# Kernel tuning notes

Measured on AMD Instinct MI355X. Metric: run time of the kernel, lower is better.

Reference implementation:

```python
import jax, jax.numpy as jnp
import numpy as np

N_USERS = 100000
N_ITEMS = 50000
N_EDGES = 1000000
D = 64


def setup_inputs() -> dict:
    key = jax.random.key(0)
    ks = jax.random.split(key, 8)
    return {
        "h_user": jax.random.normal(ks[0], (N_USERS, D), dtype=jnp.float32),
        "h_item": jax.random.normal(ks[1], (N_ITEMS, D), dtype=jnp.float32),
        "buy_src": jax.random.randint(ks[2], (N_EDGES,), 0, N_USERS),
        "buy_dst": jax.random.randint(ks[3], (N_EDGES,), 0, N_ITEMS),
        "w_buy": jax.random.uniform(ks[4], (N_EDGES,), dtype=jnp.float32),
        "bought_src": jax.random.randint(ks[5], (N_EDGES,), 0, N_ITEMS),
        "bought_dst": jax.random.randint(ks[6], (N_EDGES,), 0, N_USERS),
        "w_bought": jax.random.uniform(ks[7], (N_EDGES,), dtype=jnp.float32),
    }


def reference(h_user, h_item, buy_src, buy_dst, w_buy, bought_src, bought_dst, w_bought):
    # 'buy' etype: user -> item. message m = h_user[src] * w, reduce sum at item dst.
    msg_buy = h_user[buy_src] * w_buy[:, None]  # [E, D]
    new_item = jax.ops.segment_sum(msg_buy, buy_dst, num_segments=h_item.shape[0])
    # 'bought' etype: item -> user. message m = h_item[src] * w, reduce sum at user dst.
    msg_bought = h_item[bought_src] * w_bought[:, None]  # [E, D]
    new_user = jax.ops.segment_sum(msg_bought, bought_dst, num_segments=h_user.shape[0])
    # multi_update_all cross-reducer 'mean' is identity here: each ntype is written
    # by exactly one etype, so mean over one contribution == the sum itself.
    return (new_user, new_item)
```

## Files before the change

### kernel.cpp

```cpp
#include <hip/hip_runtime.h>


#define DIM 64

#define RB2     64
#define CAP_I   2048
#define CAP_U   1024
#define NBLK_FC 256

#define RB   128
#define CAP  4096
#define NBLK 256

__global__ void zero_u32(unsigned* __restrict__ p, int n) {
    int i = blockIdx.x * blockDim.x + threadIdx.x;
    if (i < n) p[i] = 0u;
}

__global__ void zero_f32(float4* __restrict__ out, long long n4) {
    long long i = (long long)blockIdx.x * blockDim.x + threadIdx.x;
    const long long stride = (long long)gridDim.x * blockDim.x;
    for (; i < n4; i += stride) out[i] = make_float4(0.f, 0.f, 0.f, 0.f);
}

__global__ void conv_bf16(const float4* __restrict__ in, uint4* __restrict__ out,
                          long long n8) {
    long long i = (long long)blockIdx.x * blockDim.x + threadIdx.x;
    const long long stride = (long long)gridDim.x * blockDim.x;
    for (; i < n8; i += stride) {
        const float4 a = in[2 * i];
        const float4 b = in[2 * i + 1];
        const unsigned* pa = (const unsigned*)&a;
        const unsigned* pb = (const unsigned*)&b;
        unsigned r[8];
        #pragma unroll
        for (int k = 0; k < 4; ++k) {
            unsigned u = pa[k];
            r[k] = (u + 0x7FFFu + ((u >> 16) & 1u)) >> 16;
        }
        #pragma unroll
        for (int k = 0; k < 4; ++k) {
            unsigned u = pb[k];
            r[4 + k] = (u + 0x7FFFu + ((u >> 16) & 1u)) >> 16;
        }
        uint4 o;
        o.x = r[0] | (r[1] << 16);
        o.y = r[2] | (r[3] << 16);
        o.z = r[4] | (r[5] << 16);
        o.w = r[6] | (r[7] << 16);
        out[i] = o;
    }
}

__global__ void scatter_both(const float* __restrict__ h_user,
                             const float* __restrict__ h_item,
                             const int* __restrict__ buy_src,
                             const int* __restrict__ buy_dst,
                             const float* __restrict__ w_buy,
                             const int* __restrict__ bought_src,
                             const int* __restrict__ bought_dst,
                             const float* __restrict__ w_bought,
                             float* __restrict__ new_user,
                             float* __restrict__ new_item,
                             int n_buy, int n_total) {
    const int lane = threadIdx.x & 63;
    const int waves_per_block = blockDim.x >> 6;
    int wid = blockIdx.x * waves_per_block + (threadIdx.x >> 6);
    const int nwaves = gridDim.x * waves_per_block;
    for (int e = wid; e < n_total; e += nwaves) {
        const float* h; const int* srcp; const int* dstp; const float* wp;
        float* outp; int idx;
        if (e < n_buy) { h = h_user; srcp = buy_src; dstp = buy_dst; wp = w_buy; outp = new_item; idx = e; }
        else { h = h_item; srcp = bought_src; dstp = bought_dst; wp = w_bought; outp = new_user; idx = e - n_buy; }
        const int s = srcp[idx];
        const int d = dstp[idx];
        const float weight = wp[idx];
        const float v = h[(long long)s * DIM + lane] * weight;
        atomicAdd(outp + (long long)d * DIM + lane, v);
    }
}


__global__ __launch_bounds__(512) void k3_fc(
        const int* __restrict__ buy_src, const int* __restrict__ buy_dst,
        const float* __restrict__ w_buy,
        const int* __restrict__ bought_src, const int* __restrict__ bought_dst,
        const float* __restrict__ w_bought,
        unsigned* __restrict__ cur, uint2* __restrict__ pay,
        int n_buy, int n_total, int g_item, int G, int chunk) {
    extern __shared__ unsigned sh[];
    for (int g = threadIdx.x; g < G; g += blockDim.x) sh[g] = 0u;
    __syncthreads();
    const int start = blockIdx.x * chunk;
    const int end = (start + chunk < n_total) ? start + chunk : n_total;
    for (int i = start + threadIdx.x; i < end; i += blockDim.x) {
        const int g = (i < n_buy) ? (buy_dst[i] >> 6)
                                  : (g_item + (bought_dst[i - n_buy] >> 6));
        atomicAdd(&sh[g], 1u);
    }
    __syncthreads();
    for (int g = threadIdx.x; g < G; g += blockDim.x) {
        const unsigned c = sh[g];
        sh[g] = c ? atomicAdd(&cur[g], c) : 0u;
    }
    __syncthreads();
    for (int i = start + threadIdx.x; i < end; i += blockDim.x) {
        int srcv, dstv; float wv; int g;
        if (i < n_buy) {
            srcv = buy_src[i]; dstv = buy_dst[i]; wv = w_buy[i];
            g = dstv >> 6;
        } else {
            const int j = i - n_buy;
            srcv = bought_src[j]; dstv = bought_dst[j]; wv = w_bought[j];
            g = g_item + (dstv >> 6);
        }
        const unsigned p = atomicAdd(&sh[g], 1u);
        size_t base; unsigned cap;
        if (g < g_item) { base = (size_t)g * CAP_I; cap = CAP_I; }
        else { base = (size_t)g_item * CAP_I + (size_t)(g - g_item) * CAP_U; cap = CAP_U; }
        if (p < cap)
            pay[base + p] = make_uint2((unsigned)srcv | ((unsigned)(dstv & (RB2 - 1)) << 17),
                                       __float_as_uint(wv));
    }
}

__device__ __forceinline__ float bf16_to_f32(unsigned u) {
    return __uint_as_float(u << 16);
}

__global__ __launch_bounds__(256, 8) void p4_bf16(
        const unsigned short* __restrict__ hb_user,
        const unsigned short* __restrict__ hb_item,
        const unsigned* __restrict__ cur, const uint2* __restrict__ pay,
        float* __restrict__ new_user, float* __restrict__ new_item,
        int g_item, int n_user_buckets, int ni_per, int nu_per,
        int n_items, int n_users) {
    __shared__ uint2 pbuf[CAP_I];
    __shared__ unsigned cnt[RB2];
    __shared__ unsigned pos[RB2];
    __shared__ unsigned rstart[RB2];

    const int xcd  = blockIdx.x & 7;
    const int slot = blockIdx.x >> 3;
    int g;
    if (xcd < 4) {
        if (slot >= ni_per) return;
        g = xcd * ni_per + slot;
        if (g >= g_item) return;
    } else {
        if (slot >= nu_per) return;
        const int gu = (xcd - 4) * nu_per + slot;
        if (gu >= n_user_buckets) return;
        g = g_item + gu;
    }

    const int lane = threadIdx.x & 63;
    const int wid  = threadIdx.x >> 6;
    const int sub  = lane >> 4;
    const int c4   = lane & 15;

    const unsigned short* hb; float* outp; int r0, nrowsb, cap; size_t pbase;
    if (g < g_item) {
        hb = hb_user; outp = new_item; r0 = g * RB2;
        nrowsb = n_items - r0; if (nrowsb > RB2) nrowsb = RB2;
        pbase = (size_t)g * CAP_I; cap = CAP_I;
    } else {
        const int gu = g - g_item;
        hb = hb_item; outp = new_user; r0 = gu * RB2;
        nrowsb = n_users - r0; if (nrowsb > RB2) nrowsb = RB2;
        pbase = (size_t)g_item * CAP_I + (size_t)gu * CAP_U; cap = CAP_U;
    }
    int m = (int)cur[g]; if (m > cap) m = cap;

    if (threadIdx.x < RB2) cnt[threadIdx.x] = 0u;
    __syncthreads();

    uint2 v[8];
    #pragma unroll
    for (int j = 0; j < 8; ++j) {
        const int t = (int)threadIdx.x + j * 256;
        if (t < m) {
            v[j] = pay[pbase + t];
            atomicAdd(&cnt[v[j].x >> 17], 1u);
        }
    }
    __syncthreads();
    if (wid == 0) {
        const unsigned x = cnt[lane];
        unsigned sc = x;
        #pragma unroll
        for (int d = 1; d < 64; d <<= 1) {
            unsigned u = __shfl_up(sc, d, 64);
            if (lane >= d) sc += u;
        }
        pos[lane]    = sc - x;
        rstart[lane] = sc - x;
    }
    __syncthreads();
    #pragma unroll
    for (int j = 0; j < 8; ++j) {
        const int t = (int)threadIdx.x + j * 256;
        if (t < m) {
            const unsigned q = atomicAdd(&pos[v[j].x >> 17], 1u);
            pbuf[q] = v[j];
        }
    }
    __syncthreads();

    for (int i = 0; i < 16; ++i) {
        const int r = wid * 16 + i;
        unsigned k = rstart[r];
        const unsigned ke = k + cnt[r];
        float4 a = make_float4(0.f, 0.f, 0.f, 0.f);
        for (; k + 8 <= ke; k += 8) {
            const uint2 pA = pbuf[k + sub];
            const uint2 pB = pbuf[k + 4 + sub];
            const ushort4 hA = *(const ushort4*)(hb + (size_t)(pA.x & 0x1FFFFu) * DIM + c4 * 4);
            const ushort4 hB = *(const ushort4*)(hb + (size_t)(pB.x & 0x1FFFFu) * DIM + c4 * 4);
            const float wA = __uint_as_float(pA.y);
            const float wB = __uint_as_float(pB.y);
            a.x += bf16_to_f32(hA.x) * wA; a.y += bf16_to_f32(hA.y) * wA;
            a.z += bf16_to_f32(hA.z) * wA; a.w += bf16_to_f32(hA.w) * wA;
            a.x += bf16_to_f32(hB.x) * wB; a.y += bf16_to_f32(hB.y) * wB;
            a.z += bf16_to_f32(hB.z) * wB; a.w += bf16_to_f32(hB.w) * wB;
        }
        for (; k < ke; k += 4) {
            const unsigned kk = k + (unsigned)sub;
            const uint2 p = pbuf[kk < ke ? kk : (ke - 1)];
            const float wgt = (kk < ke) ? __uint_as_float(p.y) : 0.f;
            const ushort4 hv = *(const ushort4*)(hb + (size_t)(p.x & 0x1FFFFu) * DIM + c4 * 4);
            a.x += bf16_to_f32(hv.x) * wgt; a.y += bf16_to_f32(hv.y) * wgt;
            a.z += bf16_to_f32(hv.z) * wgt; a.w += bf16_to_f32(hv.w) * wgt;
        }
        a.x += __shfl_xor(a.x, 16, 64); a.y += __shfl_xor(a.y, 16, 64);
        a.z += __shfl_xor(a.z, 16, 64); a.w += __shfl_xor(a.w, 16, 64);
        a.x += __shfl_xor(a.x, 32, 64); a.y += __shfl_xor(a.y, 32, 64);
        a.z += __shfl_xor(a.z, 32, 64); a.w += __shfl_xor(a.w, 32, 64);
        if (lane < 16 && r < nrowsb)
            *((float4*)(outp + (size_t)(r0 + r) * DIM) + c4) = a;
    }
}

__global__ __launch_bounds__(512) void k1_hist(const int* __restrict__ buy_dst,
                                               const int* __restrict__ bought_dst,
                                               unsigned* __restrict__ cnt,
                                               int n_buy, int n_total,
                                               int g_item, int G, int chunk) {
    extern __shared__ unsigned lcnt[];
    for (int g = threadIdx.x; g < G; g += blockDim.x) lcnt[g] = 0u;
    __syncthreads();
    const int start = blockIdx.x * chunk;
    const int end = (start + chunk < n_total) ? start + chunk : n_total;
    for (int i = start + threadIdx.x; i < end; i += blockDim.x) {
        const int g = (i < n_buy) ? (buy_dst[i] >> 7)
                                  : (g_item + (bought_dst[i - n_buy] >> 7));
        atomicAdd(&lcnt[g], 1u);
    }
    __syncthreads();
    for (int g = threadIdx.x; g < G; g += blockDim.x) {
        const unsigned c = lcnt[g];
        if (c) atomicAdd(&cnt[g], c);
    }
}

__global__ __launch_bounds__(64) void k2_scan(const unsigned* __restrict__ cnt,
                                              unsigned* __restrict__ starts,
                                              unsigned* __restrict__ cur, int G) {
    const int lane = threadIdx.x;
    unsigned carry = 0;
    for (int base = 0; base < G; base += 64) {
        const int i = base + lane;
        const unsigned x = (i < G) ? cnt[i] : 0u;
        unsigned sc = x;
        #pragma unroll
        for (int d = 1; d < 64; d <<= 1) {
            unsigned u = __shfl_up(sc, d, 64);
            if (lane >= d) sc += u;
        }
        const unsigned tot = __shfl(sc, 63, 64);
        if (i < G) { starts[i] = carry + sc - x; cur[i] = carry + sc - x; }
        carry += tot;
    }
}

__global__ __launch_bounds__(512) void k3_scatter(
        const int* __restrict__ buy_src, const int* __restrict__ buy_dst,
        const float* __restrict__ w_buy,
        const int* __restrict__ bought_src, const int* __restrict__ bought_dst,
        const float* __restrict__ w_bought,
        unsigned* __restrict__ cur, uint2* __restrict__ pay,
        int n_buy, int n_total, int g_item, int G, int chunk) {
    extern __shared__ unsigned sh[];
    for (int g = threadIdx.x; g < G; g += blockDim.x) sh[g] = 0u;
    __syncthreads();
    const int start = blockIdx.x * chunk;
    const int end = (start + chunk < n_total) ? start + chunk : n_total;
    for (int i = start + threadIdx.x; i < end; i += blockDim.x) {
        const int g = (i < n_buy) ? (buy_dst[i] >> 7)
                                  : (g_item + (bought_dst[i - n_buy] >> 7));
        atomicAdd(&sh[g], 1u);
    }
    __syncthreads();
    for (int g = threadIdx.x; g < G; g += blockDim.x) {
        const unsigned c = sh[g];
        sh[g] = c ? atomicAdd(&cur[g], c) : 0u;
    }
    __syncthreads();
    for (int i = start + threadIdx.x; i < end; i += blockDim.x) {
        int srcv, dstv; float wv; int g;
        if (i < n_buy) {
            srcv = buy_src[i]; dstv = buy_dst[i]; wv = w_buy[i];
            g = dstv >> 7;
        } else {
            const int j = i - n_buy;
            srcv = bought_src[j]; dstv = bought_dst[j]; wv = w_bought[j];
            g = g_item + (dstv >> 7);
        }
        const unsigned pos = atomicAdd(&sh[g], 1u);
        pay[pos] = make_uint2((unsigned)srcv | ((unsigned)(dstv & (RB - 1)) << 17),
                              __float_as_uint(wv));
    }
}

__global__ __launch_bounds__(512) void p4_sortreduce(
        const float* __restrict__ h_user, const float* __restrict__ h_item,
        const unsigned* __restrict__ starts, const uint2* __restrict__ pay,
        float* __restrict__ new_user, float* __restrict__ new_item,
        int g_item, int G, int n_items, int n_users, int n_total) {
    __shared__ uint2 pbuf[CAP];
    __shared__ unsigned cnt[RB];
    __shared__ unsigned pos[RB];
    __shared__ unsigned rstart[RB];

    const int g = blockIdx.x;
    const int lane = threadIdx.x & 63;
    const int wid  = threadIdx.x >> 6;

    const float* h; float* outp; int r0, nrows;
    if (g < g_item) { h = h_user; outp = new_item; r0 = g * RB;
                      nrows = (n_items - r0 < RB) ? n_items - r0 : RB; }
    else            { h = h_item; outp = new_user; r0 = (g - g_item) * RB;
                      nrows = (n_users - r0 < RB) ? n_users - r0 : RB; }

    const unsigned base = starts[g];
    const unsigned endp = (g + 1 < G) ? starts[g + 1] : (unsigned)n_total;

    float acc[16];
    #pragma unroll
    for (int i = 0; i < 16; ++i) acc[i] = 0.f;

    for (unsigned cbase = base; cbase < endp; cbase += CAP) {
        const unsigned rem = endp - cbase;
        const int m = (rem < (unsigned)CAP) ? (int)rem : CAP;

        for (int r = threadIdx.x; r < RB; r += blockDim.x) cnt[r] = 0u;
        __syncthreads();
        for (int t = threadIdx.x; t < m; t += blockDim.x) {
            const uint2 p = pay[cbase + t];
            atomicAdd(&cnt[p.x >> 17], 1u);
        }
        __syncthreads();
        if (wid == 0) {
            unsigned carry = 0;
            #pragma unroll
            for (int b = 0; b < RB; b += 64) {
                const unsigned x = cnt[b + lane];
                unsigned sc = x;
                #pragma unroll
                for (int d = 1; d < 64; d <<= 1) {
                    unsigned u = __shfl_up(sc, d, 64);
                    if (lane >= d) sc += u;
                }
                pos[b + lane]    = carry + sc - x;
                rstart[b + lane] = carry + sc - x;
                carry += __shfl(sc, 63, 64);
            }
        }
        __syncthreads();
        for (int t = threadIdx.x; t < m; t += blockDim.x) {
            const uint2 p = pay[cbase + t];
            const unsigned q = atomicAdd(&pos[p.x >> 17], 1u);
            pbuf[q] = p;
        }
        __syncthreads();
        #pragma unroll
        for (int i = 0; i < 16; ++i) {
            const int r = wid * 16 + i;
            unsigned k = rstart[r];
            const unsigned ke = k + cnt[r];
            float a = acc[i];
            for (; k + 4 <= ke; k += 4) {
                const uint2 p0 = pbuf[k + 0];
                const uint2 p1 = pbuf[k + 1];
                const uint2 p2 = pbuf[k + 2];
                const uint2 p3 = pbuf[k + 3];
                const float v0 = h[(size_t)(p0.x & 0x1FFFFu) * DIM + lane];
                const float v1 = h[(size_t)(p1.x & 0x1FFFFu) * DIM + lane];
                const float v2 = h[(size_t)(p2.x & 0x1FFFFu) * DIM + lane];
                const float v3 = h[(size_t)(p3.x & 0x1FFFFu) * DIM + lane];
                a += v0 * __uint_as_float(p0.y);
                a += v1 * __uint_as_float(p1.y);
                a += v2 * __uint_as_float(p2.y);
                a += v3 * __uint_as_float(p3.y);
            }
            for (; k < ke; ++k) {
                const uint2 p = pbuf[k];
                a += h[(size_t)(p.x & 0x1FFFFu) * DIM + lane] * __uint_as_float(p.y);
            }
            acc[i] = a;
        }
        __syncthreads();
    }

    #pragma unroll
    for (int i = 0; i < 16; ++i) {
        const int r = wid * 16 + i;
        if (r < nrows) outp[(size_t)(r0 + r) * DIM + lane] = acc[i];
    }
}

extern "C" void kernel_launch(void* const* d_in, const int* in_sizes, int n_in,
                              void* d_out, int out_size, void* d_ws, size_t ws_size,
                              hipStream_t stream) {
    const float* h_user     = (const float*)d_in[0];
    const float* h_item     = (const float*)d_in[1];
    const int*   buy_src    = (const int*)d_in[2];
    const int*   buy_dst    = (const int*)d_in[3];
    const float* w_buy      = (const float*)d_in[4];
    const int*   bought_src = (const int*)d_in[5];
    const int*   bought_dst = (const int*)d_in[6];
    const float* w_bought   = (const float*)d_in[7];

    const int n_users  = in_sizes[0] / DIM;
    const int n_items  = in_sizes[1] / DIM;
    const int n_buy    = in_sizes[2];
    const int n_bought = in_sizes[5];
    const int n_total  = n_buy + n_bought;

    float* out      = (float*)d_out;
    float* new_user = out;
    float* new_item = out + (long long)n_users * DIM;

    char* w = (char*)d_ws;
    size_t used = 0;
    auto alloc = [&](size_t bytes) -> char* {
        char* p = w + used;
        used += (bytes + 255) & ~(size_t)255;
        return p;
    };

    {
        const int G_ITEM = (n_items + RB2 - 1) / RB2;
        const int G_USER = (n_users + RB2 - 1) / RB2;
        const int G      = G_ITEM + G_USER;
        const size_t pay_slots = (size_t)G_ITEM * CAP_I + (size_t)G_USER * CAP_U;
        used = 0;
        unsigned*       cur = (unsigned*)alloc((size_t)G * 4);
        uint2*          pay = (uint2*)alloc(pay_slots * 8);
        unsigned short* hb  = (unsigned short*)alloc((size_t)(n_users + n_items) * DIM * 2);
        if (used <= ws_size) {
            unsigned short* hb_user = hb;
            unsigned short* hb_item = hb + (size_t)n_users * DIM;
            const int chunk = (n_total + NBLK_FC - 1) / NBLK_FC;
            const size_t smem_g = (size_t)G * 4;

            const long long n8_user = (long long)n_users * DIM / 8;
            const long long n8_item = (long long)n_items * DIM / 8;
            conv_bf16<<<2048, 256, 0, stream>>>((const float4*)h_user,
                                                (uint4*)hb_user, n8_user);
            conv_bf16<<<1024, 256, 0, stream>>>((const float4*)h_item,
                                                (uint4*)hb_item, n8_item);

            zero_u32<<<(G + 255) / 256, 256, 0, stream>>>(cur, G);
            k3_fc<<<NBLK_FC, 512, smem_g, stream>>>(buy_src, buy_dst, w_buy,
                                                    bought_src, bought_dst, w_bought,
                                                    cur, pay,
                                                    n_buy, n_total, G_ITEM, G, chunk);
            const int ni_per = (G_ITEM + 3) / 4;
            const int nu_per = (G_USER + 3) / 4;
            const int maxper = (ni_per > nu_per) ? ni_per : nu_per;
            const int grid   = 8 * maxper;
            p4_bf16<<<grid, 256, 0, stream>>>(hb_user, hb_item, cur, pay,
                                              new_user, new_item,
                                              G_ITEM, G_USER, ni_per, nu_per,
                                              n_items, n_users);
            return;
        }
    }

    {
        const int G_ITEM = (n_items + RB - 1) / RB;
        const int G_USER = (n_users + RB - 1) / RB;
        const int G      = G_ITEM + G_USER;
        used = 0;
        unsigned* cnt    = (unsigned*)alloc((size_t)G * 4);
        unsigned* starts = (unsigned*)alloc((size_t)G * 4);
        unsigned* cur    = (unsigned*)alloc((size_t)G * 4);
        uint2*    pay    = (uint2*)alloc((size_t)n_total * 8);
        if (used <= ws_size) {
            const int chunk = (n_total + NBLK - 1) / NBLK;
            const size_t smem_g = (size_t)G * 4;
            zero_u32<<<(G + 255) / 256, 256, 0, stream>>>(cnt, G);
            k1_hist<<<NBLK, 512, smem_g, stream>>>(buy_dst, bought_dst, cnt,
                                                   n_buy, n_total, G_ITEM, G, chunk);
            k2_scan<<<1, 64, 0, stream>>>(cnt, starts, cur, G);
            k3_scatter<<<NBLK, 512, smem_g, stream>>>(buy_src, buy_dst, w_buy,
                                                      bought_src, bought_dst, w_bought,
                                                      cur, pay,
                                                      n_buy, n_total, G_ITEM, G, chunk);
            p4_sortreduce<<<G, 512, 0, stream>>>(h_user, h_item, starts, pay,
                                                 new_user, new_item,
                                                 G_ITEM, G, n_items, n_users, n_total);
            return;
        }
    }

    const long long n4 = (long long)out_size / 4;
    zero_f32<<<2048, 256, 0, stream>>>((float4*)d_out, n4);
    scatter_both<<<2048, 256, 0, stream>>>(h_user, h_item,
                                           buy_src, buy_dst, w_buy,
                                           bought_src, bought_dst, w_bought,
                                           new_user, new_item,
                                           n_buy, n_total);
}
```

Measured before the change: 92.06 us.

## Replace atomic bucket reservation with per-block count matrix and column scan

The fused count-and-scatter kernel, which reserved bucket offsets with global atomics across 256 blocks, is split into three kernels. A count pass writes per-block histograms into a 1024×G uint16 matrix, a wave-per-column scan turns them into exclusive offsets and totals, and a scatter pass loads its row as starting offsets. This spreads the work over more blocks with deterministic placement and no global atomic contention. The cost is two extra launches plus a roughly 3 MB count matrix that is written, scanned and read back.

```diff
diff --git a/kernel.cpp b/kernel.cpp
--- a/kernel.cpp
+++ b/kernel.cpp
@@ -6,7 +6,7 @@
 #define RB2     64
 #define CAP_I   2048
 #define CAP_U   1024
-#define NBLK_FC 256
+#define NBM     1024
 
 #define RB   128
 #define CAP  4096
@@ -81,12 +81,9 @@
 }
 
 
-__global__ __launch_bounds__(512) void k3_fc(
-        const int* __restrict__ buy_src, const int* __restrict__ buy_dst,
-        const float* __restrict__ w_buy,
-        const int* __restrict__ bought_src, const int* __restrict__ bought_dst,
-        const float* __restrict__ w_bought,
-        unsigned* __restrict__ cur, uint2* __restrict__ pay,
+__global__ __launch_bounds__(256) void p1m(
+        const int* __restrict__ buy_dst, const int* __restrict__ bought_dst,
+        unsigned short* __restrict__ cnt_m,
         int n_buy, int n_total, int g_item, int G, int chunk) {
     extern __shared__ unsigned sh[];
     for (int g = threadIdx.x; g < G; g += blockDim.x) sh[g] = 0u;
@@ -99,25 +96,62 @@
         atomicAdd(&sh[g], 1u);
     }
     __syncthreads();
-    for (int g = threadIdx.x; g < G; g += blockDim.x) {
-        const unsigned c = sh[g];
-        sh[g] = c ? atomicAdd(&cur[g], c) : 0u;
-    }
-    __syncthreads();
+    unsigned short* row = cnt_m + (size_t)blockIdx.x * G;
+    for (int g = threadIdx.x; g < G; g += blockDim.x)
+        row[g] = (unsigned short)(sh[g] > 0xFFFFu ? 0xFFFFu : sh[g]);
+}
+
+__global__ __launch_bounds__(256) void s_col(
+        unsigned short* __restrict__ cnt_m, unsigned* __restrict__ cur,
+        int G, int nbm) {
+    const int col = blockIdx.x * (blockDim.x >> 6) + ((int)threadIdx.x >> 6);
+    if (col >= G) return;
+    const int lane = threadIdx.x & 63;
+    unsigned carry = 0;
+    for (int base = 0; base < nbm; base += 64) {
+        const int b = base + lane;
+        const size_t idx = (size_t)b * G + col;
+        const unsigned x = cnt_m[idx];
+        unsigned sc = x;
+        #pragma unroll
+        for (int d = 1; d < 64; d <<= 1) {
+            unsigned u = __shfl_up(sc, d, 64);
+            if (lane >= d) sc += u;
+        }
+        const unsigned tot = __shfl(sc, 63, 64);
+        const unsigned excl = carry + sc - x;
+        cnt_m[idx] = (unsigned short)(excl > 0xFFFFu ? 0xFFFFu : excl);
+        carry += tot;
+    }
+    if (lane == 0) cur[col] = carry;
+}
+
+__global__ __launch_bounds__(256) void p3m(
+        const int* __restrict__ buy_src, const int* __restrict__ buy_dst,
+        const float* __restrict__ w_buy,
+        const int* __restrict__ bought_src, const int* __restrict__ bought_dst,
+        const float* __restrict__ w_bought,
+        const unsigned short* __restrict__ cnt_m, uint2* __restrict__ pay,
+        int n_buy, int n_total, int g_item, int G, int chunk) {
+    extern __shared__ unsigned sh[];
+    const unsigned short* row = cnt_m + (size_t)blockIdx.x * G;
+    for (int g = threadIdx.x; g < G; g += blockDim.x) sh[g] = row[g];
+    __syncthreads();
+    const int start = blockIdx.x * chunk;
+    const int end = (start + chunk < n_total) ? start + chunk : n_total;
     for (int i = start + threadIdx.x; i < end; i += blockDim.x) {
-        int srcv, dstv; float wv; int g;
+        int srcv, dstv; float wv; int g; size_t base; unsigned cap;
         if (i < n_buy) {
             srcv = buy_src[i]; dstv = buy_dst[i]; wv = w_buy[i];
             g = dstv >> 6;
+            base = (size_t)g * CAP_I; cap = CAP_I;
         } else {
             const int j = i - n_buy;
             srcv = bought_src[j]; dstv = bought_dst[j]; wv = w_bought[j];
             g = g_item + (dstv >> 6);
+            base = (size_t)g_item * CAP_I + (size_t)(g - g_item) * CAP_U; cap = CAP_U;
         }
         const unsigned p = atomicAdd(&sh[g], 1u);
-        size_t base; unsigned cap;
-        if (g < g_item) { base = (size_t)g * CAP_I; cap = CAP_I; }
-        else { base = (size_t)g_item * CAP_I + (size_t)(g - g_item) * CAP_U; cap = CAP_U; }
         if (p < cap)
             pay[base + p] = make_uint2((unsigned)srcv | ((unsigned)(dstv & (RB2 - 1)) << 17),
                                        __float_as_uint(wv));
@@ -455,13 +489,14 @@
         const int G      = G_ITEM + G_USER;
         const size_t pay_slots = (size_t)G_ITEM * CAP_I + (size_t)G_USER * CAP_U;
         used = 0;
-        unsigned*       cur = (unsigned*)alloc((size_t)G * 4);
-        uint2*          pay = (uint2*)alloc(pay_slots * 8);
-        unsigned short* hb  = (unsigned short*)alloc((size_t)(n_users + n_items) * DIM * 2);
+        unsigned*       cur   = (unsigned*)alloc((size_t)G * 4);
+        unsigned short* cnt_m = (unsigned short*)alloc((size_t)NBM * G * 2);
+        uint2*          pay   = (uint2*)alloc(pay_slots * 8);
+        unsigned short* hb    = (unsigned short*)alloc((size_t)(n_users + n_items) * DIM * 2);
         if (used <= ws_size) {
             unsigned short* hb_user = hb;
             unsigned short* hb_item = hb + (size_t)n_users * DIM;
-            const int chunk = (n_total + NBLK_FC - 1) / NBLK_FC;
+            const int chunk = (n_total + NBM - 1) / NBM;
             const size_t smem_g = (size_t)G * 4;
 
             const long long n8_user = (long long)n_users * DIM / 8;
@@ -471,11 +506,15 @@
             conv_bf16<<<1024, 256, 0, stream>>>((const float4*)h_item,
                                                 (uint4*)hb_item, n8_item);
 
-            zero_u32<<<(G + 255) / 256, 256, 0, stream>>>(cur, G);
-            k3_fc<<<NBLK_FC, 512, smem_g, stream>>>(buy_src, buy_dst, w_buy,
-                                                    bought_src, bought_dst, w_bought,
-                                                    cur, pay,
-                                                    n_buy, n_total, G_ITEM, G, chunk);
+            p1m<<<NBM, 256, smem_g, stream>>>(buy_dst, bought_dst, cnt_m,
+                                              n_buy, n_total, G_ITEM, G, chunk);
+            const int scol_grid = (G + 3) / 4;
+            s_col<<<scol_grid, 256, 0, stream>>>(cnt_m, cur, G, NBM);
+            p3m<<<NBM, 256, smem_g, stream>>>(buy_src, buy_dst, w_buy,
+                                              bought_src, bought_dst, w_bought,
+                                              cnt_m, pay,
+                                              n_buy, n_total, G_ITEM, G, chunk);
+
             const int ni_per = (G_ITEM + 3) / 4;
             const int nu_per = (G_USER + 3) / 4;
             const int maxper = (ni_per > nu_per) ? ni_per : nu_per;
```

Result: slower. 122.1 us (+32.7%).

## Shard bucket counters and payload slots to spread binning across more blocks

Applied to the files above, without the earlier changes.

The binning kernel now launches 2048 blocks instead of 256, split by edge type. Each bucket's global cursor and payload region is divided into 16 shards chosen by block index, which is meant to cut contention on the global atomics. The gather kernel reads the 16 shard counters and loads up to 16 payload entries per thread, with occupancy lowered to 6. In exchange, each block still zeroes and scans the full per-bucket shared histogram, so zeroing and scan work grows eightfold. Per-shard capacities of 144 and 72 risk silently dropping edges if a shard overflows.

```diff
diff --git a/kernel.cpp b/kernel.cpp
--- a/kernel.cpp
+++ b/kernel.cpp
@@ -4,9 +4,13 @@
 #define DIM 64
 
 #define RB2     64
-#define CAP_I   2048
-#define CAP_U   1024
-#define NBLK_FC 256
+#define SH      16
+#define SCAP_I  144
+#define SCAP_U  72
+#define CAP_I   (SH * SCAP_I)
+#define CAP_U   (SH * SCAP_U)
+#define TCAP    2048
+#define NBH     1024
 
 #define RB   128
 #define CAP  4096
@@ -87,40 +91,48 @@
         const int* __restrict__ bought_src, const int* __restrict__ bought_dst,
         const float* __restrict__ w_bought,
         unsigned* __restrict__ cur, uint2* __restrict__ pay,
-        int n_buy, int n_total, int g_item, int G, int chunk) {
+        int n_buy, int n_bought, int g_item, int G) {
     extern __shared__ unsigned sh[];
     for (int g = threadIdx.x; g < G; g += blockDim.x) sh[g] = 0u;
     __syncthreads();
-    const int start = blockIdx.x * chunk;
-    const int end = (start + chunk < n_total) ? start + chunk : n_total;
-    for (int i = start + threadIdx.x; i < end; i += blockDim.x) {
-        const int g = (i < n_buy) ? (buy_dst[i] >> 6)
-                                  : (g_item + (bought_dst[i - n_buy] >> 6));
-        atomicAdd(&sh[g], 1u);
-    }
-    __syncthreads();
+
+    const int b = blockIdx.x;
+    const int shard = b & (SH - 1);
+    const bool is_buy = (b < NBH);
+    const int bh = is_buy ? b : (b - NBH);
+    const int n_e = is_buy ? n_buy : n_bought;
+    const int chunk = (n_e + NBH - 1) / NBH;
+    const int start = bh * chunk;
+    const int end = (start + chunk < n_e) ? start + chunk : n_e;
+    const int step = blockDim.x;
+    const int* __restrict__ dstp = is_buy ? buy_dst : bought_dst;
+    const int* __restrict__ srcp = is_buy ? buy_src : bought_src;
+    const float* __restrict__ wp = is_buy ? w_buy : w_bought;
+    const int gofs = is_buy ? 0 : g_item;
+
+    for (int i = start + (int)threadIdx.x; i < end; i += step)
+        atomicAdd(&sh[gofs + (dstp[i] >> 6)], 1u);
+    __syncthreads();
+
     for (int g = threadIdx.x; g < G; g += blockDim.x) {
         const unsigned c = sh[g];
-        sh[g] = c ? atomicAdd(&cur[g], c) : 0u;
-    }
-    __syncthreads();
-    for (int i = start + threadIdx.x; i < end; i += blockDim.x) {
-        int srcv, dstv; float wv; int g;
-        if (i < n_buy) {
-            srcv = buy_src[i]; dstv = buy_dst[i]; wv = w_buy[i];
-            g = dstv >> 6;
-        } else {
-            const int j = i - n_buy;
-            srcv = bought_src[j]; dstv = bought_dst[j]; wv = w_bought[j];
-            g = g_item + (dstv >> 6);
-        }
+        sh[g] = c ? atomicAdd(&cur[(size_t)g * SH + shard], c) : 0u;
+    }
+    __syncthreads();
+
+    for (int i = start + (int)threadIdx.x; i < end; i += step) {
+        const int srcv = srcp[i];
+        const int dstv = dstp[i];
+        const float wv = wp[i];
+        const int g = gofs + (dstv >> 6);
         const unsigned p = atomicAdd(&sh[g], 1u);
-        size_t base; unsigned cap;
-        if (g < g_item) { base = (size_t)g * CAP_I; cap = CAP_I; }
-        else { base = (size_t)g_item * CAP_I + (size_t)(g - g_item) * CAP_U; cap = CAP_U; }
-        if (p < cap)
-            pay[base + p] = make_uint2((unsigned)srcv | ((unsigned)(dstv & (RB2 - 1)) << 17),
-                                       __float_as_uint(wv));
+        size_t base; unsigned scap;
+        if (is_buy) { base = (size_t)g * CAP_I; scap = SCAP_I; }
+        else { base = (size_t)g_item * CAP_I + (size_t)(g - g_item) * CAP_U; scap = SCAP_U; }
+        if (p < scap)
+            pay[base + (size_t)shard * scap + p] =
+                make_uint2((unsigned)srcv | ((unsigned)(dstv & (RB2 - 1)) << 17),
+                           __float_as_uint(wv));
     }
 }
 
@@ -128,14 +140,14 @@
     return __uint_as_float(u << 16);
 }
 
-__global__ __launch_bounds__(256, 8) void p4_bf16(
+__global__ __launch_bounds__(256, 6) void p4_bf16(
         const unsigned short* __restrict__ hb_user,
         const unsigned short* __restrict__ hb_item,
         const unsigned* __restrict__ cur, const uint2* __restrict__ pay,
         float* __restrict__ new_user, float* __restrict__ new_item,
         int g_item, int n_user_buckets, int ni_per, int nu_per,
         int n_items, int n_users) {
-    __shared__ uint2 pbuf[CAP_I];
+    __shared__ uint2 pbuf[TCAP];
     __shared__ unsigned cnt[RB2];
     __shared__ unsigned pos[RB2];
     __shared__ unsigned rstart[RB2];
@@ -154,34 +166,37 @@
         g = g_item + gu;
     }
 
-    const int lane = threadIdx.x & 63;
-    const int wid  = threadIdx.x >> 6;
+    const int tid  = threadIdx.x;
+    const int lane = tid & 63;
+    const int wid  = tid >> 6;
     const int sub  = lane >> 4;
     const int c4   = lane & 15;
 
-    const unsigned short* hb; float* outp; int r0, nrowsb, cap; size_t pbase;
+    const unsigned short* hb; float* outp; int r0, nrowsb; unsigned scap; size_t pbase;
     if (g < g_item) {
         hb = hb_user; outp = new_item; r0 = g * RB2;
         nrowsb = n_items - r0; if (nrowsb > RB2) nrowsb = RB2;
-        pbase = (size_t)g * CAP_I; cap = CAP_I;
+        pbase = (size_t)g * CAP_I; scap = SCAP_I;
     } else {
         const int gu = g - g_item;
         hb = hb_item; outp = new_user; r0 = gu * RB2;
         nrowsb = n_users - r0; if (nrowsb > RB2) nrowsb = RB2;
-        pbase = (size_t)g_item * CAP_I + (size_t)gu * CAP_U; cap = CAP_U;
-    }
-    int m = (int)cur[g]; if (m > cap) m = cap;
-
-    if (threadIdx.x < RB2) cnt[threadIdx.x] = 0u;
-    __syncthreads();
-
-    uint2 v[8];
+        pbase = (size_t)g_item * CAP_I + (size_t)gu * CAP_U; scap = SCAP_U;
+    }
+
+    if (tid < RB2) cnt[tid] = 0u;
+    __syncthreads();
+
+    uint2 v[SH];
+    unsigned vmask = 0;
     #pragma unroll
-    for (int j = 0; j < 8; ++j) {
-        const int t = (int)threadIdx.x + j * 256;
-        if (t < m) {
-            v[j] = pay[pbase + t];
-            atomicAdd(&cnt[v[j].x >> 17], 1u);
+    for (int s = 0; s < SH; ++s) {
+        unsigned c = cur[(size_t)g * SH + s];
+        if (c > scap) c = scap;
+        if ((unsigned)tid < c) {
+            v[s] = pay[pbase + (size_t)s * scap + tid];
+            vmask |= 1u << s;
+            atomicAdd(&cnt[v[s].x >> 17], 1u);
         }
     }
     __syncthreads();
@@ -198,11 +213,10 @@
     }
     __syncthreads();
     #pragma unroll
-    for (int j = 0; j < 8; ++j) {
-        const int t = (int)threadIdx.x + j * 256;
-        if (t < m) {
-            const unsigned q = atomicAdd(&pos[v[j].x >> 17], 1u);
-            pbuf[q] = v[j];
+    for (int s = 0; s < SH; ++s) {
+        if (vmask & (1u << s)) {
+            const unsigned q = atomicAdd(&pos[v[s].x >> 17], 1u);
+            if (q < TCAP) pbuf[q] = v[s];
         }
     }
     __syncthreads();
@@ -455,13 +469,12 @@
         const int G      = G_ITEM + G_USER;
         const size_t pay_slots = (size_t)G_ITEM * CAP_I + (size_t)G_USER * CAP_U;
         used = 0;
-        unsigned*       cur = (unsigned*)alloc((size_t)G * 4);
+        unsigned*       cur = (unsigned*)alloc((size_t)G * SH * 4);
         uint2*          pay = (uint2*)alloc(pay_slots * 8);
         unsigned short* hb  = (unsigned short*)alloc((size_t)(n_users + n_items) * DIM * 2);
         if (used <= ws_size) {
             unsigned short* hb_user = hb;
             unsigned short* hb_item = hb + (size_t)n_users * DIM;
-            const int chunk = (n_total + NBLK_FC - 1) / NBLK_FC;
             const size_t smem_g = (size_t)G * 4;
 
             const long long n8_user = (long long)n_users * DIM / 8;
@@ -471,11 +484,12 @@
             conv_bf16<<<1024, 256, 0, stream>>>((const float4*)h_item,
                                                 (uint4*)hb_item, n8_item);
 
-            zero_u32<<<(G + 255) / 256, 256, 0, stream>>>(cur, G);
-            k3_fc<<<NBLK_FC, 512, smem_g, stream>>>(buy_src, buy_dst, w_buy,
+            zero_u32<<<(G * SH + 255) / 256, 256, 0, stream>>>(cur, G * SH);
+            k3_fc<<<2 * NBH, 512, smem_g, stream>>>(buy_src, buy_dst, w_buy,
                                                     bought_src, bought_dst, w_bought,
                                                     cur, pay,
-                                                    n_buy, n_total, G_ITEM, G, chunk);
+                                                    n_buy, n_bought, G_ITEM, G);
+
             const int ni_per = (G_ITEM + 3) / 4;
             const int nu_per = (G_USER + 3) / 4;
             const int maxper = (ni_per > nu_per) ? ni_per : nu_per;
```

After: 147.8 us. 60.6% more time.
